# Optimization experiments

Measured on AMD Instinct MI355X. Metric: run time of the kernel, lower is better.

## Reference

```python
import jax, jax.numpy as jnp
import numpy as np

B, T = 128, 512
V, E, H, A, L = 50000, 256, 512, 64, 2


def setup_inputs() -> dict:
    key = jax.random.key(0)
    ks = jax.random.split(key, 16)
    token_ids = jax.random.randint(ks[0], (B, T), 0, V, dtype=jnp.int32)
    # lengths must be >= 2 so that the source's (len-1)-1 index is valid
    lengths = jnp.clip(jax.random.randint(ks[1], (B,), 0, T, dtype=jnp.int32), 4, T)
    s = 0.05
    inp = {
        "token_ids": token_ids,
        "lengths": lengths,
        "embedding": jax.random.normal(ks[2], (V, E), jnp.float32) * s,
        "Wt": jax.random.normal(ks[3], (A, E), jnp.float32) * s,   # tokens_linear
        "bt": jax.random.normal(ks[4], (A,), jnp.float32) * s,
        "Wq": jax.random.normal(ks[5], (A, H), jnp.float32) * s,   # query_linear
        "bq": jax.random.normal(ks[6], (A,), jnp.float32) * s,
        "v": jax.random.normal(ks[7], (A,), jnp.float32) * s,      # attention_linear weight
        "bv": jax.random.normal(ks[8], (), jnp.float32) * s,       # attention_linear bias
        "gru_Wih0": jax.random.normal(ks[9], (3 * H, A), jnp.float32) * s,
        "gru_Whh0": jax.random.normal(ks[10], (3 * H, H), jnp.float32) * s,
        "gru_bih0": jax.random.normal(ks[11], (3 * H,), jnp.float32) * s,
        "gru_bhh0": jax.random.normal(ks[12], (3 * H,), jnp.float32) * s,
        "gru_Wih1": jax.random.normal(ks[13], (3 * H, H), jnp.float32) * s,
        "gru_Whh1": jax.random.normal(ks[14], (3 * H, H), jnp.float32) * s,
        "gru_bih1": jax.random.normal(ks[15], (3 * H,), jnp.float32) * s,
        "gru_bhh1": jax.random.normal(jax.random.fold_in(key, 99), (3 * H,), jnp.float32) * s,
    }
    return inp


def _gru_cell(x, h, Wih, Whh, bih, bhh):
    gi = x @ Wih.T + bih      # [B, 3H]
    gh = h @ Whh.T + bhh      # [B, 3H]
    i_r, i_z, i_n = jnp.split(gi, 3, axis=-1)
    h_r, h_z, h_n = jnp.split(gh, 3, axis=-1)
    r = jax.nn.sigmoid(i_r + h_r)
    z = jax.nn.sigmoid(i_z + h_z)
    n = jnp.tanh(i_n + r * h_n)
    return (1.0 - z) * n + z * h


def reference(token_ids, lengths, embedding, Wt, bt, Wq, bq, v, bv,
              gru_Wih0, gru_Whh0, gru_bih0, gru_bhh0,
              gru_Wih1, gru_Whh1, gru_bih1, gru_bhh1):
    x = embedding[token_ids]                 # [B, T, E]
    tp = jnp.einsum('bte,ae->bta', x, Wt) + bt   # tokens_linear, [B, T, A]
    pos = jnp.arange(T)

    def step(h, i):
        # query = hidden_state[-1] (zeros at step 0, matching hidden_state=None)
        q = h[-1] @ Wq.T + bq                # [B, A]
        s = jnp.tanh(tp + q[:, None, :]) @ v + bv   # [B, T]
        s = jnp.where(pos[None, :] <= i, s, -jnp.inf)  # growing prefix
        attn = jax.nn.softmax(s, axis=1)
        ctx = jnp.einsum('bt,bta->ba', attn, tp)     # [B, A]
        h0 = _gru_cell(ctx, h[0], gru_Wih0, gru_Whh0, gru_bih0, gru_bhh0)
        h1 = _gru_cell(h0, h[1], gru_Wih1, gru_Whh1, gru_bih1, gru_bhh1)
        return jnp.stack([h0, h1]), h1

    h_init = jnp.zeros((L, B, H), tp.dtype)
    _, outs = jax.lax.scan(step, h_init, jnp.arange(T))   # outs: [T, B, H]
    # source: sequence_lengths = len-1, then index sequence_lengths-1 = len-2
    idx = jnp.clip(lengths - 2, 0, T - 1)
    result = outs[idx, jnp.arange(B)]                     # [B, H]
    return result
```

## Files before the change

kernel.cpp:

```cpp
#include <hip/hip_runtime.h>

#define NB 128
#define NT 512
#define NE 256
#define NH 512
#define NA 64
#define NG 8
#define WPG 32
#define GB 16

typedef short bf16x8 __attribute__((ext_vector_type(8)));
typedef float f32x4 __attribute__((ext_vector_type(4)));
typedef unsigned short u16x8 __attribute__((ext_vector_type(8)));
typedef unsigned long long u64;

__device__ __forceinline__ unsigned short f2bf(float f){
  unsigned u = __builtin_bit_cast(unsigned, f);
  u = u + 0x7fffu + ((u >> 16) & 1u);
  return (unsigned short)(u >> 16);
}
__device__ __forceinline__ float bf2f(unsigned short h){
  unsigned u = ((unsigned)h) << 16;
  return __builtin_bit_cast(float, u);
}
__device__ __forceinline__ bf16x8 packbf2(f32x4 a, f32x4 b){
  bf16x8 r;
  r[0]=(short)f2bf(a[0]); r[1]=(short)f2bf(a[1]); r[2]=(short)f2bf(a[2]); r[3]=(short)f2bf(a[3]);
  r[4]=(short)f2bf(b[0]); r[5]=(short)f2bf(b[1]); r[6]=(short)f2bf(b[2]); r[7]=(short)f2bf(b[3]);
  return r;
}
__device__ __forceinline__ bf16x8 loadB_f32(const float* p){
  f32x4 a = *(const f32x4*)p;
  f32x4 b = *(const f32x4*)(p + 4);
  return packbf2(a, b);
}
#define MFMA(a,b,c) __builtin_amdgcn_mfma_f32_16x16x32_bf16(a,b,c,0,0,0)

__device__ __forceinline__ float fsig(float x){
  return __builtin_amdgcn_rcpf(1.f + __expf(-x));
}
__device__ __forceinline__ float ftanh(float x){
  float e2 = __expf(2.f * x);
  return 1.f - 2.f * __builtin_amdgcn_rcpf(e2 + 1.f);
}

struct fpair { float x, y; };
__device__ __forceinline__ fpair aload_f2(const float* p){
  u64 u = __hip_atomic_load((const u64*)p, __ATOMIC_RELAXED, __HIP_MEMORY_SCOPE_AGENT);
  fpair r;
  r.x = __builtin_bit_cast(float, (unsigned)u);
  r.y = __builtin_bit_cast(float, (unsigned)(u >> 32));
  return r;
}
__device__ __forceinline__ float aload_f(const float* p){
  return __hip_atomic_load(p, __ATOMIC_RELAXED, __HIP_MEMORY_SCOPE_AGENT);
}
__device__ __forceinline__ u64 astore_bf4r(unsigned short* p, f32x4 x){
  union { unsigned short s[4]; u64 u; } t;
  t.s[0]=f2bf(x[0]); t.s[1]=f2bf(x[1]); t.s[2]=f2bf(x[2]); t.s[3]=f2bf(x[3]);
  return __hip_atomic_exchange((u64*)p, t.u, __ATOMIC_RELAXED, __HIP_MEMORY_SCOPE_AGENT);
}
__device__ __forceinline__ u64 azero8r(u64* p){
  return __hip_atomic_exchange(p, 0ull, __ATOMIC_RELAXED, __HIP_MEMORY_SCOPE_AGENT);
}
__device__ __forceinline__ float afaddr(float* p, float v){
  return __hip_atomic_fetch_add(p, v, __ATOMIC_RELAXED, __HIP_MEMORY_SCOPE_AGENT);
}

__global__ __launch_bounds__(256) void k_tp(
    const int* __restrict__ tok, const float* __restrict__ emb,
    const float* __restrict__ Wt, const float* __restrict__ bt,
    unsigned short* __restrict__ tp)
{
  const int lane = threadIdx.x & 63;
  const int w = threadIdx.x >> 6;
  const int m16 = lane & 15, quad = lane >> 4;

  bf16x8 wfq[8][4];
#pragma unroll
  for (int kc = 0; kc < 8; kc++)
#pragma unroll
    for (int nt = 0; nt < 4; nt++)
      wfq[kc][nt] = loadB_f32(Wt + (nt*16 + m16)*NE + kc*32 + quad*8);

  float btv[4];
#pragma unroll
  for (int nt = 0; nt < 4; nt++) btv[nt] = bt[nt*16 + m16];

  const int gw = blockIdx.x * 4 + w;
#pragma unroll 1
  for (int it = 0; it < 4; it++){
    const int pt = gw * 4 + it;
    const int pos = pt*16 + m16;
    const long row = (long)tok[pos];
    const float* xrow = emb + row * NE;
    f32x4 acc[4] = {{0,0,0,0},{0,0,0,0},{0,0,0,0},{0,0,0,0}};
#pragma unroll
    for (int kc = 0; kc < 8; kc++){
      bf16x8 af = loadB_f32(xrow + kc*32 + quad*8);
#pragma unroll
      for (int nt = 0; nt < 4; nt++)
        acc[nt] = MFMA(af, wfq[kc][nt], acc[nt]);
    }
#pragma unroll
    for (int nt = 0; nt < 4; nt++)
#pragma unroll
      for (int r = 0; r < 4; r++){
        int posr = pt*16 + quad*4 + r;
        tp[(long)posr * NA + nt*16 + m16] = f2bf(acc[nt][r] + btv[nt]);
      }
  }
}

__global__ __launch_bounds__(256) void k_pack(
    const float* __restrict__ Wq, unsigned short* __restrict__ blob)
{
  const int lane = threadIdx.x & 63, wv = threadIdx.x >> 6;
  const int m16 = lane & 15, quad = lane >> 4;
#pragma unroll
  for (int kc = 0; kc < 16; kc++){
    bf16x8 t = loadB_f32(Wq + (long)(wv*16 + m16)*NH + kc*32 + quad*8);
    *(bf16x8*)&blob[((wv*16 + kc)*64 + lane)*8] = t;
  }
}

struct KArgs {
  const int* len;
  const float* bq; const float* v; const float* bv;
  const float* Wih0; const float* Whh0; const float* bih0; const float* bhh0;
  const float* Wih1; const float* Whh1; const float* bih1; const float* bhh1;
  const unsigned short* tp;
  const unsigned short* wqblob;
  unsigned short* h0b; unsigned short* h1b;
  float* ctxg; float* deng;
  int* ctrl;
  float* out;
};

__device__ __forceinline__ void gbar(int* cnt, int& ep){
  __syncthreads();
  ep++;
  if (threadIdx.x == 0){
    __hip_atomic_fetch_add(cnt, 1, __ATOMIC_RELAXED, __HIP_MEMORY_SCOPE_AGENT);
    const int tgt = WPG * ep;
    while (__hip_atomic_load(cnt, __ATOMIC_RELAXED, __HIP_MEMORY_SCOPE_AGENT) < tgt)
      __builtin_amdgcn_s_sleep(1);
  }
  __syncthreads();
}

__device__ __forceinline__ void stage_h(const unsigned short* hb,
                                        unsigned short (*hs)[64][8], int tid){
  const int lane = tid & 63, wv = tid >> 6;
  const int b = lane & 15, quad = lane >> 4;
#pragma unroll
  for (int c = 0; c < 4; c++){
    const int kc = wv*4 + c;
    const unsigned short* src = hb + b*NH + kc*32 + quad*8;
    union { u64 u[2]; bf16x8 v; } t;
    t.u[0] = __hip_atomic_load((const u64*)src,     __ATOMIC_RELAXED, __HIP_MEMORY_SCOPE_AGENT);
    t.u[1] = __hip_atomic_load((const u64*)(src+4), __ATOMIC_RELAXED, __HIP_MEMORY_SCOPE_AGENT);
    *(bf16x8*)&hs[kc][lane][0] = t.v;
  }
}

__global__ __launch_bounds__(256, 1) void k_main(KArgs A_)
{
  const int tid = threadIdx.x, lane = tid & 63, w = tid >> 6;
  const int g = blockIdx.x & 7, m = blockIdx.x >> 3;
  const int m16 = lane & 15, quad = lane >> 4;

  __shared__ __attribute__((aligned(16))) unsigned short h0s[16][64][8];
  __shared__ __attribute__((aligned(16))) unsigned short h1s[16][64][8];
  __shared__ __attribute__((aligned(16))) float dslab[6][256];
  __shared__ __attribute__((aligned(16))) float qs[16][68];

  unsigned short* h0b = A_.h0b + g * GB * NH;
  unsigned short* h1b = A_.h1b + g * GB * NH;
  float* ctxg = A_.ctxg + g * GB * NA;
  float* deng = A_.deng + g * GB;
  int* bar    = A_.ctrl + g * 64;
  const int b0 = g * GB;

  u64  usink = 0;
  float fsink = 0.f;

  bf16x8 wf[48], wih0f[2];
  float bhh0v[4], bih0v[4], bhh1v[4], bih1v[4];
  if (w < 3){
    const int r0 = w * NH + m * 16;
#pragma unroll
    for (int kc = 0; kc < 16; kc++){
      wf[kc]    = loadB_f32(A_.Whh0 + (long)(r0 + m16)*NH + kc*32 + quad*8);
      wf[16+kc] = loadB_f32(A_.Whh1 + (long)(r0 + m16)*NH + kc*32 + quad*8);
      wf[32+kc] = loadB_f32(A_.Wih1 + (long)(r0 + m16)*NH + kc*32 + quad*8);
    }
#pragma unroll
    for (int kc = 0; kc < 2; kc++)
      wih0f[kc] = loadB_f32(A_.Wih0 + (r0 + m16)*NA + kc*32 + quad*8);
#pragma unroll
    for (int r = 0; r < 4; r++){
      int d = r0 + quad*4 + r;
      bhh0v[r] = A_.bhh0[d]; bih0v[r] = A_.bih0[d];
      bhh1v[r] = A_.bhh1[d]; bih1v[r] = A_.bih1[d];
    }
  }
  float bqw[4];
#pragma unroll
  for (int r = 0; r < 4; r++) bqw[r] = A_.bq[w*16 + quad*4 + r];

  float vv[16];
#pragma unroll
  for (int jj = 0; jj < 16; jj++) vv[jj] = A_.v[quad*16 + jj];
  const float bvv = A_.bv[0];
  const int gwav = m*4 + w;
  const int ab = gwav & 15;
  const int wr = gwav >> 4;

  f32x4 h0p = {0,0,0,0}, h1p = {0,0,0,0};
  if (w == 3){
    f32x4 z = {0,0,0,0};
    usink += astore_bf4r(&h0b[m16*NH + m*16 + quad*4], z);
    usink += astore_bf4r(&h1b[m16*NH + m*16 + quad*4], z);
  }
  if (w == 1){
    if (lane < 16) usink += azero8r((u64*)ctxg + m*16 + lane);
    if (lane == 16 && m < 8) usink += azero8r((u64*)deng + m);
  }

  int myidx = 0, imax = 0;
#pragma unroll 1
  for (int b = 0; b < GB; b++){
    int L = A_.len[b0 + b];
    int ix = L - 2; ix = ix < 0 ? 0 : (ix > NT-1 ? NT-1 : ix);
    if (b == m16) myidx = ix;
    imax = imax > ix ? imax : ix;
  }

  int ep = 0;
  gbar(bar, ep);

  f32x4 gh0c = {0,0,0,0};
  if (w < 3){
#pragma unroll
    for (int r = 0; r < 4; r++) gh0c[r] = bhh0v[r];
  }

#pragma unroll 1
  for (int i = 0; i <= imax; i++){
    stage_h(h1b, h1s, tid);
    __syncthreads();

    f32x4 gh1 = {0,0,0,0};
    {
      f32x4 qa = {0,0,0,0};
      if (w < 3){
#pragma unroll
        for (int kc = 0; kc < 16; kc++){
          bf16x8 b1f = *(const bf16x8*)&h1s[kc][lane][0];
          gh1 = MFMA(wf[16+kc], b1f, gh1);
          bf16x8 af = *(const bf16x8*)&A_.wqblob[((w*16 + kc)*64 + lane)*8];
          qa = MFMA(af, b1f, qa);
        }
#pragma unroll
        for (int r = 0; r < 4; r++) gh1[r] += bhh1v[r];
      } else {
#pragma unroll
        for (int kc = 0; kc < 16; kc++){
          bf16x8 b1f = *(const bf16x8*)&h1s[kc][lane][0];
          bf16x8 af = *(const bf16x8*)&A_.wqblob[((w*16 + kc)*64 + lane)*8];
          qa = MFMA(af, b1f, qa);
        }
      }
#pragma unroll
      for (int r = 0; r < 4; r++)
        qs[m16][w*16 + quad*4 + r] = qa[r] + bqw[r];
    }
    __syncthreads();

    float qv[16];
#pragma unroll
    for (int jq = 0; jq < 4; jq++){
      f32x4 t = *(const f32x4*)&qs[ab][quad*16 + jq*4];
      qv[jq*4+0]=t[0]; qv[jq*4+1]=t[1]; qv[jq*4+2]=t[2]; qv[jq*4+3]=t[3];
    }
    float ctxp[16];
#pragma unroll
    for (int jj = 0; jj < 16; jj++) ctxp[jj] = 0.f;
    float denp = 0.f;
    const unsigned short* tpb = A_.tp + (long)(b0 + ab) * NT * NA;
#pragma unroll 1
    for (int c = wr; c*16 <= i; c += 8){
      const int t = c*16 + m16;
      const unsigned short* tpp = tpb + (long)t*NA + quad*16;
      u16x8 ta = *(const u16x8*)tpp;
      u16x8 tb = *(const u16x8*)(tpp + 8);
      float tpf[16];
#pragma unroll
      for (int jj = 0; jj < 8; jj++){ tpf[jj] = bf2f(ta[jj]); tpf[8+jj] = bf2f(tb[jj]); }
      float sp = 0.f;
#pragma unroll
      for (int jj = 0; jj < 16; jj++){
        float x = tpf[jj] + qv[jj];
        sp = fmaf(ftanh(x), vv[jj], sp);
      }
      sp += __shfl_xor(sp, 16);
      sp += __shfl_xor(sp, 32);
      float e = __expf(sp + bvv);
      e = (t <= i) ? e : 0.f;
      denp += e;
#pragma unroll
      for (int jj = 0; jj < 16; jj++) ctxp[jj] = fmaf(e, tpf[jj], ctxp[jj]);
    }
#pragma unroll
    for (int off = 1; off < 64; off <<= 1) denp += __shfl_xor(denp, off);
    denp *= 0.25f;
#pragma unroll
    for (int st = 0; st < 4; st++){
      const int bit = 1 << st;
      const bool up = (lane >> st) & 1;
      const int n2 = (16 >> st) >> 1;
#pragma unroll
      for (int j2 = 0; j2 < 8; j2++){
        if (j2 < n2){
          float keep = up ? ctxp[2*j2+1] : ctxp[2*j2];
          float send = up ? ctxp[2*j2]   : ctxp[2*j2+1];
          float got = __shfl_xor(send, bit);
          ctxp[j2] = keep + got;
        }
      }
    }
    fsink += afaddr(&ctxg[ab*NA + lane], ctxp[0]);
    if (lane == 0) fsink += afaddr(&deng[ab], denp);

    gbar(bar, ep);

    if (w < 3){
      f32x4 gi0 = {0,0,0,0};
      const float rdn = 1.0f / aload_f(&deng[m16]);
#pragma unroll
      for (int kc = 0; kc < 2; kc++){
        const float* cp = &ctxg[m16*NA + kc*32 + quad*8];
        f32x4 c0, c1;
        fpair p0 = aload_f2(cp+0); c0[0]=p0.x; c0[1]=p0.y;
        fpair p1 = aload_f2(cp+2); c0[2]=p1.x; c0[3]=p1.y;
        fpair p2 = aload_f2(cp+4); c1[0]=p2.x; c1[1]=p2.y;
        fpair p3 = aload_f2(cp+6); c1[2]=p3.x; c1[3]=p3.y;
#pragma unroll
        for (int r = 0; r < 4; r++){ c0[r] *= rdn; c1[r] *= rdn; }
        gi0 = MFMA(wih0f[kc], packbf2(c0, c1), gi0);
      }
#pragma unroll
      for (int r = 0; r < 4; r++) gi0[r] += bih0v[r];
      *(f32x4*)&dslab[w][lane*4] = gh0c;
      *(f32x4*)&dslab[3+w][lane*4] = gi0;
    }
    __syncthreads();
    if (w == 3){
      f32x4 ghr = *(f32x4*)&dslab[0][lane*4];
      f32x4 ghz = *(f32x4*)&dslab[1][lane*4];
      f32x4 ghn = *(f32x4*)&dslab[2][lane*4];
      f32x4 gir = *(f32x4*)&dslab[3][lane*4];
      f32x4 giz = *(f32x4*)&dslab[4][lane*4];
      f32x4 gin = *(f32x4*)&dslab[5][lane*4];
      f32x4 hn;
#pragma unroll
      for (int r = 0; r < 4; r++){
        float rr = fsig(gir[r] + ghr[r]);
        float zz = fsig(giz[r] + ghz[r]);
        float nn = ftanh(gin[r] + rr*ghn[r]);
        hn[r] = (1.f - zz)*nn + zz*h0p[r];
      }
      h0p = hn;
      usink += astore_bf4r(&h0b[m16*NH + m*16 + quad*4], hn);
    }
    gbar(bar, ep);

    stage_h(h0b, h0s, tid);
    __syncthreads();
    if (w < 3){
      f32x4 gi1 = {0,0,0,0}, g0 = {0,0,0,0};
#pragma unroll
      for (int kc = 0; kc < 16; kc++){
        bf16x8 hf = *(const bf16x8*)&h0s[kc][lane][0];
        gi1 = MFMA(wf[32+kc], hf, gi1);
        g0  = MFMA(wf[kc],    hf, g0);
      }
#pragma unroll
      for (int r = 0; r < 4; r++){ gi1[r] += bih1v[r]; g0[r] += bhh0v[r]; }
      gh0c = g0;
      *(f32x4*)&dslab[w][lane*4] = gh1;
      *(f32x4*)&dslab[3+w][lane*4] = gi1;
    }
    if (w == 1){
      if (lane < 16) usink += azero8r((u64*)ctxg + m*16 + lane);
      if (lane == 16 && m < 8) usink += azero8r((u64*)deng + m);
    }
    __syncthreads();
    if (w == 3){
      f32x4 ghr = *(f32x4*)&dslab[0][lane*4];
      f32x4 ghz = *(f32x4*)&dslab[1][lane*4];
      f32x4 ghn = *(f32x4*)&dslab[2][lane*4];
      f32x4 gir = *(f32x4*)&dslab[3][lane*4];
      f32x4 giz = *(f32x4*)&dslab[4][lane*4];
      f32x4 gin = *(f32x4*)&dslab[5][lane*4];
      f32x4 hn;
#pragma unroll
      for (int r = 0; r < 4; r++){
        float rr = fsig(gir[r] + ghr[r]);
        float zz = fsig(giz[r] + ghz[r]);
        float nn = ftanh(gin[r] + rr*ghn[r]);
        hn[r] = (1.f - zz)*nn + zz*h1p[r];
      }
      h1p = hn;
      usink += astore_bf4r(&h1b[m16*NH + m*16 + quad*4], hn);
      if (i == myidx)
        *(f32x4*)&A_.out[(long)(b0 + m16)*NH + m*16 + quad*4] = hn;
    }
    gbar(bar, ep);
  }

  u64 total = usink + (u64)__builtin_bit_cast(unsigned, fsink);
  if (total == 0x9e3779b97f4a7c15ull && A_.len[0] == -12345)
    A_.ctrl[56 + g] = (int)total;
}

extern "C" void kernel_launch(void* const* d_in, const int* in_sizes, int n_in,
                              void* d_out, int out_size, void* d_ws, size_t ws_size,
                              hipStream_t stream)
{
  (void)in_sizes; (void)n_in; (void)out_size; (void)ws_size;
  char* ws = (char*)d_ws;
  unsigned short* tp  = (unsigned short*)ws;
  unsigned short* h0b = (unsigned short*)(ws + 8388608);
  unsigned short* h1b = h0b + NB*NH;
  float* ctxg = (float*)(h1b + NB*NH);
  float* deng = ctxg + NB*NA;
  int* ctrl   = (int*)((char*)deng + 4096);
  unsigned short* wqblob = (unsigned short*)((char*)ctrl + 2048);

  (void)hipMemsetAsync(ctrl, 0, 2048, stream);

  k_tp<<<dim3(256), dim3(256), 0, stream>>>(
      (const int*)d_in[0], (const float*)d_in[2], (const float*)d_in[3],
      (const float*)d_in[4], tp);
  k_pack<<<dim3(1), dim3(256), 0, stream>>>((const float*)d_in[5], wqblob);

  KArgs ka;
  ka.len  = (const int*)d_in[1];
  ka.bq   = (const float*)d_in[6];
  ka.v    = (const float*)d_in[7];  ka.bv   = (const float*)d_in[8];
  ka.Wih0 = (const float*)d_in[9];  ka.Whh0 = (const float*)d_in[10];
  ka.bih0 = (const float*)d_in[11]; ka.bhh0 = (const float*)d_in[12];
  ka.Wih1 = (const float*)d_in[13]; ka.Whh1 = (const float*)d_in[14];
  ka.bih1 = (const float*)d_in[15]; ka.bhh1 = (const float*)d_in[16];
  ka.tp = tp; ka.wqblob = wqblob; ka.h0b = h0b; ka.h1b = h1b;
  ka.ctxg = ctxg; ka.deng = deng; ka.ctrl = ctrl; ka.out = (float*)d_out;

  k_main<<<dim3(256), dim3(256), 0, stream>>>(ka);
}
```

Baseline: 7.742 ms.

## Replace group barriers with sequence-tagged flag-in-data polling and double buffering

Drops the counter-based group barrier and the atomic-add context reduction. Every hidden-state and context value is now published as a 64-bit word holding a step sequence number next to the payload. Consumers spin on those tags, with hidden and context buffers double-buffered by step parity. The attention partial sums are reduced in shared memory first and published by only two blocks per batch row instead of accumulated with atomics. The Whh0 matmul is moved so it overlaps the context wait, aiming to remove barrier latency on the serial recurrence path at the cost of more polling traffic and larger buffer words.

```diff
diff --git a/kernel.cpp b/kernel.cpp
--- a/kernel.cpp
+++ b/kernel.cpp
@@ -6,7 +6,6 @@
 #define NH 512
 #define NA 64
 #define NG 8
-#define WPG 32
 #define GB 16
 
 typedef short bf16x8 __attribute__((ext_vector_type(8)));
@@ -44,27 +43,17 @@
   return 1.f - 2.f * __builtin_amdgcn_rcpf(e2 + 1.f);
 }
 
-struct fpair { float x, y; };
-__device__ __forceinline__ fpair aload_f2(const float* p){
-  u64 u = __hip_atomic_load((const u64*)p, __ATOMIC_RELAXED, __HIP_MEMORY_SCOPE_AGENT);
-  fpair r;
-  r.x = __builtin_bit_cast(float, (unsigned)u);
-  r.y = __builtin_bit_cast(float, (unsigned)(u >> 32));
-  return r;
-}
-__device__ __forceinline__ float aload_f(const float* p){
+__device__ __forceinline__ u64 aload(const u64* p){
   return __hip_atomic_load(p, __ATOMIC_RELAXED, __HIP_MEMORY_SCOPE_AGENT);
 }
-__device__ __forceinline__ u64 astore_bf4r(unsigned short* p, f32x4 x){
-  union { unsigned short s[4]; u64 u; } t;
-  t.s[0]=f2bf(x[0]); t.s[1]=f2bf(x[1]); t.s[2]=f2bf(x[2]); t.s[3]=f2bf(x[3]);
-  return __hip_atomic_exchange((u64*)p, t.u, __ATOMIC_RELAXED, __HIP_MEMORY_SCOPE_AGENT);
-}
-__device__ __forceinline__ u64 azero8r(u64* p){
-  return __hip_atomic_exchange(p, 0ull, __ATOMIC_RELAXED, __HIP_MEMORY_SCOPE_AGENT);
-}
-__device__ __forceinline__ float afaddr(float* p, float v){
-  return __hip_atomic_fetch_add(p, v, __ATOMIC_RELAXED, __HIP_MEMORY_SCOPE_AGENT);
+__device__ __forceinline__ void fire(u64* p, u64 v){
+  (void)__hip_atomic_exchange(p, v, __ATOMIC_RELAXED, __HIP_MEMORY_SCOPE_AGENT);
+}
+__device__ __forceinline__ u64 packh(unsigned sq, float a, float b){
+  return ((u64)sq << 32) | ((u64)f2bf(b) << 16) | (u64)f2bf(a);
+}
+__device__ __forceinline__ u64 packf(unsigned sq, float a){
+  return ((u64)sq << 32) | (u64)__builtin_bit_cast(unsigned, a);
 }
 
 __global__ __launch_bounds__(256) void k_tp(
@@ -131,36 +120,33 @@
   const float* Wih1; const float* Whh1; const float* bih1; const float* bhh1;
   const unsigned short* tp;
   const unsigned short* wqblob;
-  unsigned short* h0b; unsigned short* h1b;
-  float* ctxg; float* deng;
-  int* ctrl;
+  u64* hbuf;
+  u64* cbuf;
   float* out;
 };
 
-__device__ __forceinline__ void gbar(int* cnt, int& ep){
-  __syncthreads();
-  ep++;
-  if (threadIdx.x == 0){
-    __hip_atomic_fetch_add(cnt, 1, __ATOMIC_RELAXED, __HIP_MEMORY_SCOPE_AGENT);
-    const int tgt = WPG * ep;
-    while (__hip_atomic_load(cnt, __ATOMIC_RELAXED, __HIP_MEMORY_SCOPE_AGENT) < tgt)
-      __builtin_amdgcn_s_sleep(1);
-  }
-  __syncthreads();
-}
-
-__device__ __forceinline__ void stage_h(const unsigned short* hb,
-                                        unsigned short (*hs)[64][8], int tid){
+__device__ __forceinline__ void stage_poll(const u64* __restrict__ buf, unsigned sq,
+                                           unsigned short (*hs)[64][8], int tid){
   const int lane = tid & 63, wv = tid >> 6;
-  const int b = lane & 15, quad = lane >> 4;
+  const int b = lane & 15, q8 = lane >> 4;
 #pragma unroll
   for (int c = 0; c < 4; c++){
     const int kc = wv*4 + c;
-    const unsigned short* src = hb + b*NH + kc*32 + quad*8;
-    union { u64 u[2]; bf16x8 v; } t;
-    t.u[0] = __hip_atomic_load((const u64*)src,     __ATOMIC_RELAXED, __HIP_MEMORY_SCOPE_AGENT);
-    t.u[1] = __hip_atomic_load((const u64*)(src+4), __ATOMIC_RELAXED, __HIP_MEMORY_SCOPE_AGENT);
-    *(bf16x8*)&hs[kc][lane][0] = t.v;
+    const u64* u0 = buf + (kc*16 + q8*4)*16 + b;
+    u64 x0, x1, x2, x3;
+    for (;;){
+      x0 = aload(u0);      x1 = aload(u0 + 16);
+      x2 = aload(u0 + 32); x3 = aload(u0 + 48);
+      if ((unsigned)(x0>>32)==sq && (unsigned)(x1>>32)==sq &&
+          (unsigned)(x2>>32)==sq && (unsigned)(x3>>32)==sq) break;
+      __builtin_amdgcn_s_sleep(1);
+    }
+    u16x8 d;
+    d[0]=(unsigned short)x0; d[1]=(unsigned short)(x0>>16);
+    d[2]=(unsigned short)x1; d[3]=(unsigned short)(x1>>16);
+    d[4]=(unsigned short)x2; d[5]=(unsigned short)(x2>>16);
+    d[6]=(unsigned short)x3; d[7]=(unsigned short)(x3>>16);
+    *(u16x8*)&hs[kc][lane][0] = d;
   }
 }
 
@@ -174,16 +160,13 @@
   __shared__ __attribute__((aligned(16))) unsigned short h1s[16][64][8];
   __shared__ __attribute__((aligned(16))) float dslab[6][256];
   __shared__ __attribute__((aligned(16))) float qs[16][68];
-
-  unsigned short* h0b = A_.h0b + g * GB * NH;
-  unsigned short* h1b = A_.h1b + g * GB * NH;
-  float* ctxg = A_.ctxg + g * GB * NA;
-  float* deng = A_.deng + g * GB;
-  int* bar    = A_.ctrl + g * 64;
+  __shared__ __attribute__((aligned(16))) float cslab[4][64];
+  __shared__ float cden[4];
+  __shared__ __attribute__((aligned(16))) unsigned short ctxf[64][16];
+
+  u64* hb = A_.hbuf + (long)g * (4*4096);
+  u64* cb = A_.cbuf + (long)g * (2*2*16*72);
   const int b0 = g * GB;
-
-  u64  usink = 0;
-  float fsink = 0.f;
 
   bf16x8 wf[48], wih0f[2];
   float bhh0v[4], bih0v[4], bhh1v[4], bih1v[4];
@@ -213,20 +196,8 @@
 #pragma unroll
   for (int jj = 0; jj < 16; jj++) vv[jj] = A_.v[quad*16 + jj];
   const float bvv = A_.bv[0];
-  const int gwav = m*4 + w;
-  const int ab = gwav & 15;
-  const int wr = gwav >> 4;
-
-  f32x4 h0p = {0,0,0,0}, h1p = {0,0,0,0};
-  if (w == 3){
-    f32x4 z = {0,0,0,0};
-    usink += astore_bf4r(&h0b[m16*NH + m*16 + quad*4], z);
-    usink += astore_bf4r(&h1b[m16*NH + m*16 + quad*4], z);
-  }
-  if (w == 1){
-    if (lane < 16) usink += azero8r((u64*)ctxg + m*16 + lane);
-    if (lane == 16 && m < 8) usink += azero8r((u64*)deng + m);
-  }
+  const int ab = m >> 1;
+  const int wr = (m & 1)*4 + w;
 
   int myidx = 0, imax = 0;
 #pragma unroll 1
@@ -237,40 +208,35 @@
     imax = imax > ix ? imax : ix;
   }
 
-  int ep = 0;
-  gbar(bar, ep);
-
-  f32x4 gh0c = {0,0,0,0};
-  if (w < 3){
-#pragma unroll
-    for (int r = 0; r < 4; r++) gh0c[r] = bhh0v[r];
-  }
+  f32x4 h0p = {0,0,0,0}, h1p = {0,0,0,0};
+
+  {
+    u16x8 z = {0,0,0,0,0,0,0,0};
+#pragma unroll
+    for (int c = 0; c < 4; c++){
+      int kc = (tid>>6)*4 + c;
+      *(u16x8*)&h0s[kc][lane][0] = z;
+      *(u16x8*)&h1s[kc][lane][0] = z;
+    }
+  }
+  __syncthreads();
 
 #pragma unroll 1
   for (int i = 0; i <= imax; i++){
-    stage_h(h1b, h1s, tid);
-    __syncthreads();
-
-    f32x4 gh1 = {0,0,0,0};
+    const int par = i & 1;
+    const unsigned sq = (unsigned)(i + 1);
+
+    if (i > 0){
+      stage_poll(hb + (long)(2 + ((i-1)&1))*4096, (unsigned)i, h1s, tid);
+      __syncthreads();
+    }
     {
       f32x4 qa = {0,0,0,0};
-      if (w < 3){
-#pragma unroll
-        for (int kc = 0; kc < 16; kc++){
-          bf16x8 b1f = *(const bf16x8*)&h1s[kc][lane][0];
-          gh1 = MFMA(wf[16+kc], b1f, gh1);
-          bf16x8 af = *(const bf16x8*)&A_.wqblob[((w*16 + kc)*64 + lane)*8];
-          qa = MFMA(af, b1f, qa);
-        }
-#pragma unroll
-        for (int r = 0; r < 4; r++) gh1[r] += bhh1v[r];
-      } else {
-#pragma unroll
-        for (int kc = 0; kc < 16; kc++){
-          bf16x8 b1f = *(const bf16x8*)&h1s[kc][lane][0];
-          bf16x8 af = *(const bf16x8*)&A_.wqblob[((w*16 + kc)*64 + lane)*8];
-          qa = MFMA(af, b1f, qa);
-        }
+#pragma unroll
+      for (int kc = 0; kc < 16; kc++){
+        bf16x8 b1f = *(const bf16x8*)&h1s[kc][lane][0];
+        bf16x8 af = *(const bf16x8*)&A_.wqblob[((w*16 + kc)*64 + lane)*8];
+        qa = MFMA(af, b1f, qa);
       }
 #pragma unroll
       for (int r = 0; r < 4; r++)
@@ -278,81 +244,126 @@
     }
     __syncthreads();
 
-    float qv[16];
-#pragma unroll
-    for (int jq = 0; jq < 4; jq++){
-      f32x4 t = *(const f32x4*)&qs[ab][quad*16 + jq*4];
-      qv[jq*4+0]=t[0]; qv[jq*4+1]=t[1]; qv[jq*4+2]=t[2]; qv[jq*4+3]=t[3];
-    }
-    float ctxp[16];
-#pragma unroll
-    for (int jj = 0; jj < 16; jj++) ctxp[jj] = 0.f;
-    float denp = 0.f;
-    const unsigned short* tpb = A_.tp + (long)(b0 + ab) * NT * NA;
+    {
+      float qv[16];
+#pragma unroll
+      for (int jq = 0; jq < 4; jq++){
+        f32x4 t = *(const f32x4*)&qs[ab][quad*16 + jq*4];
+        qv[jq*4+0]=t[0]; qv[jq*4+1]=t[1]; qv[jq*4+2]=t[2]; qv[jq*4+3]=t[3];
+      }
+      float ctxp[16];
+#pragma unroll
+      for (int jj = 0; jj < 16; jj++) ctxp[jj] = 0.f;
+      float denp = 0.f;
+      const unsigned short* tpb = A_.tp + (long)(b0 + ab) * NT * NA;
 #pragma unroll 1
-    for (int c = wr; c*16 <= i; c += 8){
-      const int t = c*16 + m16;
-      const unsigned short* tpp = tpb + (long)t*NA + quad*16;
-      u16x8 ta = *(const u16x8*)tpp;
-      u16x8 tb = *(const u16x8*)(tpp + 8);
-      float tpf[16];
-#pragma unroll
-      for (int jj = 0; jj < 8; jj++){ tpf[jj] = bf2f(ta[jj]); tpf[8+jj] = bf2f(tb[jj]); }
-      float sp = 0.f;
-#pragma unroll
-      for (int jj = 0; jj < 16; jj++){
-        float x = tpf[jj] + qv[jj];
-        sp = fmaf(ftanh(x), vv[jj], sp);
-      }
-      sp += __shfl_xor(sp, 16);
-      sp += __shfl_xor(sp, 32);
-      float e = __expf(sp + bvv);
-      e = (t <= i) ? e : 0.f;
-      denp += e;
-#pragma unroll
-      for (int jj = 0; jj < 16; jj++) ctxp[jj] = fmaf(e, tpf[jj], ctxp[jj]);
-    }
-#pragma unroll
-    for (int off = 1; off < 64; off <<= 1) denp += __shfl_xor(denp, off);
-    denp *= 0.25f;
-#pragma unroll
-    for (int st = 0; st < 4; st++){
-      const int bit = 1 << st;
-      const bool up = (lane >> st) & 1;
-      const int n2 = (16 >> st) >> 1;
-#pragma unroll
-      for (int j2 = 0; j2 < 8; j2++){
-        if (j2 < n2){
-          float keep = up ? ctxp[2*j2+1] : ctxp[2*j2];
-          float send = up ? ctxp[2*j2]   : ctxp[2*j2+1];
-          float got = __shfl_xor(send, bit);
-          ctxp[j2] = keep + got;
+      for (int c = wr; c*16 <= i; c += 8){
+        const int t = c*16 + m16;
+        const unsigned short* tpp = tpb + (long)t*NA + quad*16;
+        u16x8 ta = *(const u16x8*)tpp;
+        u16x8 tb = *(const u16x8*)(tpp + 8);
+        float tpf[16];
+#pragma unroll
+        for (int jj = 0; jj < 8; jj++){ tpf[jj] = bf2f(ta[jj]); tpf[8+jj] = bf2f(tb[jj]); }
+        float sp = 0.f;
+#pragma unroll
+        for (int jj = 0; jj < 16; jj++){
+          float x = tpf[jj] + qv[jj];
+          sp = fmaf(ftanh(x), vv[jj], sp);
         }
-      }
-    }
-    fsink += afaddr(&ctxg[ab*NA + lane], ctxp[0]);
-    if (lane == 0) fsink += afaddr(&deng[ab], denp);
-
-    gbar(bar, ep);
-
+        sp += __shfl_xor(sp, 16);
+        sp += __shfl_xor(sp, 32);
+        float e = __expf(sp + bvv);
+        e = (t <= i) ? e : 0.f;
+        denp += e;
+#pragma unroll
+        for (int jj = 0; jj < 16; jj++) ctxp[jj] = fmaf(e, tpf[jj], ctxp[jj]);
+      }
+#pragma unroll
+      for (int off = 1; off < 64; off <<= 1) denp += __shfl_xor(denp, off);
+      denp *= 0.25f;
+#pragma unroll
+      for (int st = 0; st < 4; st++){
+        const int bit = 1 << st;
+        const bool up = (lane >> st) & 1;
+        const int n2 = (16 >> st) >> 1;
+#pragma unroll
+        for (int j2 = 0; j2 < 8; j2++){
+          if (j2 < n2){
+            float keep = up ? ctxp[2*j2+1] : ctxp[2*j2];
+            float send = up ? ctxp[2*j2]   : ctxp[2*j2+1];
+            float got = __shfl_xor(send, bit);
+            ctxp[j2] = keep + got;
+          }
+        }
+      }
+      cslab[w][lane] = ctxp[0];
+      if (lane == 0) cden[w] = denp;
+    }
+    __syncthreads();
+    if (w == 0){
+      float s = cslab[0][lane] + cslab[1][lane] + cslab[2][lane] + cslab[3][lane];
+      u64* slot = cb + ((long)(par*2 + (m & 1))*16 + ab)*72;
+      fire(slot + lane, packf(sq, s));
+      if (lane == 0)
+        fire(slot + 64, packf(sq, cden[0]+cden[1]+cden[2]+cden[3]));
+    }
+
+    f32x4 gh1 = {0,0,0,0}, g0 = {0,0,0,0};
+    if (w < 3){
+#pragma unroll
+      for (int kc = 0; kc < 16; kc++){
+        bf16x8 b1f = *(const bf16x8*)&h1s[kc][lane][0];
+        gh1 = MFMA(wf[16+kc], b1f, gh1);
+        bf16x8 h0f = *(const bf16x8*)&h0s[kc][lane][0];
+        g0  = MFMA(wf[kc], h0f, g0);
+      }
+#pragma unroll
+      for (int r = 0; r < 4; r++){ gh1[r] += bhh1v[r]; g0[r] += bhh0v[r]; }
+    } else {
+      const u64* c0 = cb + ((long)(par*2 + 0)*16 + m16)*72;
+      const u64* c1 = cb + ((long)(par*2 + 1)*16 + m16)*72;
+      u64 d0, d1;
+      for (;;){
+        d0 = aload(c0 + 64); d1 = aload(c1 + 64);
+        if ((unsigned)(d0>>32)==sq && (unsigned)(d1>>32)==sq) break;
+        __builtin_amdgcn_s_sleep(1);
+      }
+      const float rdn = __builtin_amdgcn_rcpf(
+          __builtin_bit_cast(float,(unsigned)d0) + __builtin_bit_cast(float,(unsigned)d1));
+#pragma unroll
+      for (int kc = 0; kc < 2; kc++){
+        const int a0 = kc*32 + quad*8;
+        u64 t0[8], t1[8];
+        for (;;){
+          bool ok = true;
+#pragma unroll
+          for (int j = 0; j < 8; j++){ t0[j] = aload(c0 + a0 + j); ok &= ((unsigned)(t0[j]>>32)==sq); }
+#pragma unroll
+          for (int j = 0; j < 8; j++){ t1[j] = aload(c1 + a0 + j); ok &= ((unsigned)(t1[j]>>32)==sq); }
+          if (ok) break;
+          __builtin_amdgcn_s_sleep(1);
+        }
+        u16x8 f;
+#pragma unroll
+        for (int j = 0; j < 8; j++){
+          float s = (__builtin_bit_cast(float,(unsigned)t0[j]) +
+                     __builtin_bit_cast(float,(unsigned)t1[j])) * rdn;
+          f[j] = f2bf(s);
+        }
+        *(u16x8*)&ctxf[lane][kc*8] = f;
+      }
+    }
+    __syncthreads();
     if (w < 3){
       f32x4 gi0 = {0,0,0,0};
-      const float rdn = 1.0f / aload_f(&deng[m16]);
-#pragma unroll
-      for (int kc = 0; kc < 2; kc++){
-        const float* cp = &ctxg[m16*NA + kc*32 + quad*8];
-        f32x4 c0, c1;
-        fpair p0 = aload_f2(cp+0); c0[0]=p0.x; c0[1]=p0.y;
-        fpair p1 = aload_f2(cp+2); c0[2]=p1.x; c0[3]=p1.y;
-        fpair p2 = aload_f2(cp+4); c1[0]=p2.x; c1[1]=p2.y;
-        fpair p3 = aload_f2(cp+6); c1[2]=p3.x; c1[3]=p3.y;
-#pragma unroll
-        for (int r = 0; r < 4; r++){ c0[r] *= rdn; c1[r] *= rdn; }
-        gi0 = MFMA(wih0f[kc], packbf2(c0, c1), gi0);
-      }
+      bf16x8 cf0 = *(const bf16x8*)&ctxf[lane][0];
+      bf16x8 cf1 = *(const bf16x8*)&ctxf[lane][8];
+      gi0 = MFMA(wih0f[0], cf0, gi0);
+      gi0 = MFMA(wih0f[1], cf1, gi0);
 #pragma unroll
       for (int r = 0; r < 4; r++) gi0[r] += bih0v[r];
-      *(f32x4*)&dslab[w][lane*4] = gh0c;
+      *(f32x4*)&dslab[w][lane*4] = g0;
       *(f32x4*)&dslab[3+w][lane*4] = gi0;
     }
     __syncthreads();
@@ -372,29 +383,24 @@
         hn[r] = (1.f - zz)*nn + zz*h0p[r];
       }
       h0p = hn;
-      usink += astore_bf4r(&h0b[m16*NH + m*16 + quad*4], hn);
-    }
-    gbar(bar, ep);
-
-    stage_h(h0b, h0s, tid);
+      u64* p0 = hb + (long)par*4096 + (m*8 + quad*2)*16 + m16;
+      fire(p0,      packh(sq, hn[0], hn[1]));
+      fire(p0 + 16, packh(sq, hn[2], hn[3]));
+    }
+
+    stage_poll(hb + (long)par*4096, sq, h0s, tid);
     __syncthreads();
     if (w < 3){
-      f32x4 gi1 = {0,0,0,0}, g0 = {0,0,0,0};
+      f32x4 gi1 = {0,0,0,0};
 #pragma unroll
       for (int kc = 0; kc < 16; kc++){
         bf16x8 hf = *(const bf16x8*)&h0s[kc][lane][0];
         gi1 = MFMA(wf[32+kc], hf, gi1);
-        g0  = MFMA(wf[kc],    hf, g0);
-      }
-#pragma unroll
-      for (int r = 0; r < 4; r++){ gi1[r] += bih1v[r]; g0[r] += bhh0v[r]; }
-      gh0c = g0;
+      }
+#pragma unroll
+      for (int r = 0; r < 4; r++) gi1[r] += bih1v[r];
       *(f32x4*)&dslab[w][lane*4] = gh1;
       *(f32x4*)&dslab[3+w][lane*4] = gi1;
-    }
-    if (w == 1){
-      if (lane < 16) usink += azero8r((u64*)ctxg + m*16 + lane);
-      if (lane == 16 && m < 8) usink += azero8r((u64*)deng + m);
     }
     __syncthreads();
     if (w == 3){
@@ -413,16 +419,13 @@
         hn[r] = (1.f - zz)*nn + zz*h1p[r];
       }
       h1p = hn;
-      usink += astore_bf4r(&h1b[m16*NH + m*16 + quad*4], hn);
+      u64* p1 = hb + (long)(2 + par)*4096 + (m*8 + quad*2)*16 + m16;
+      fire(p1,      packh(sq, hn[0], hn[1]));
+      fire(p1 + 16, packh(sq, hn[2], hn[3]));
       if (i == myidx)
         *(f32x4*)&A_.out[(long)(b0 + m16)*NH + m*16 + quad*4] = hn;
     }
-    gbar(bar, ep);
-  }
-
-  u64 total = usink + (u64)__builtin_bit_cast(unsigned, fsink);
-  if (total == 0x9e3779b97f4a7c15ull && A_.len[0] == -12345)
-    A_.ctrl[56 + g] = (int)total;
+  }
 }
 
 extern "C" void kernel_launch(void* const* d_in, const int* in_sizes, int n_in,
@@ -431,15 +434,12 @@
 {
   (void)in_sizes; (void)n_in; (void)out_size; (void)ws_size;
   char* ws = (char*)d_ws;
-  unsigned short* tp  = (unsigned short*)ws;
-  unsigned short* h0b = (unsigned short*)(ws + 8388608);
-  unsigned short* h1b = h0b + NB*NH;
-  float* ctxg = (float*)(h1b + NB*NH);
-  float* deng = ctxg + NB*NA;
-  int* ctrl   = (int*)((char*)deng + 4096);
-  unsigned short* wqblob = (unsigned short*)((char*)ctrl + 2048);
-
-  (void)hipMemsetAsync(ctrl, 0, 2048, stream);
+  unsigned short* tp     = (unsigned short*)ws;
+  unsigned short* wqblob = (unsigned short*)(ws + 8388608);
+  u64* hbuf = (u64*)(ws + 8388608 + 65536);
+  u64* cbuf = hbuf + 8 * (4*4096);
+
+  (void)hipMemsetAsync(hbuf, 0xFF, (size_t)(8*4*4096 + 8*2*2*16*72) * sizeof(u64), stream);
 
   k_tp<<<dim3(256), dim3(256), 0, stream>>>(
       (const int*)d_in[0], (const float*)d_in[2], (const float*)d_in[3],
@@ -454,8 +454,9 @@
   ka.bih0 = (const float*)d_in[11]; ka.bhh0 = (const float*)d_in[12];
   ka.Wih1 = (const float*)d_in[13]; ka.Whh1 = (const float*)d_in[14];
   ka.bih1 = (const float*)d_in[15]; ka.bhh1 = (const float*)d_in[16];
-  ka.tp = tp; ka.wqblob = wqblob; ka.h0b = h0b; ka.h1b = h1b;
-  ka.ctxg = ctxg; ka.deng = deng; ka.ctrl = ctrl; ka.out = (float*)d_out;
+  ka.tp = tp; ka.wqblob = wqblob;
+  ka.hbuf = hbuf; ka.cbuf = cbuf;
+  ka.out = (float*)d_out;
 
   k_main<<<dim3(256), dim3(256), 0, stream>>>(ka);
 }
```

Result: faster. 7.063 ms (-8.8%).
